# Optimization experiments

Hardware: AMD Instinct MI355X
Metric: run time of the kernel (lower is better)

The kernel has to match this reference:

```python
import jax, jax.numpy as jnp
import numpy as np

V, E, F, K, Y = 50000, 128, 256, 3, 1000  # vocab, embed, filters, kernel, labels


def setup_inputs() -> dict:
    key = jax.random.key(0)
    ks = jax.random.split(key, 8)
    x = jax.random.randint(ks[0], (16, 4096), 0, V)
    target = jax.random.randint(ks[1], (16,), 0, Y)
    embed_w = jax.random.normal(ks[2], (V, E), dtype=jnp.float32) * 0.02
    embed_w = embed_w.at[0].set(0.0)  # padding_idx=0
    conv_w = jax.random.normal(ks[3], (F, E, K), dtype=jnp.float32) * (1.0 / np.sqrt(E * K))
    conv_b = jnp.zeros((F,), dtype=jnp.float32)
    U_w = jax.random.normal(ks[4], (Y, F), dtype=jnp.float32) * (1.0 / np.sqrt(F))
    fc_w = jax.random.normal(ks[5], (Y, F), dtype=jnp.float32) * (1.0 / np.sqrt(F))
    fc_b = jnp.zeros((Y,), dtype=jnp.float32)
    return {"x": x, "target": target, "embed_w": embed_w, "conv_w": conv_w,
            "conv_b": conv_b, "U_w": U_w, "fc_w": fc_w, "fc_b": fc_b}


def reference(x, target, embed_w, conv_w, conv_b, U_w, fc_w, fc_b):
    # embedding lookup: (B, L, E); dropout is identity in eval mode
    h = embed_w[x]
    h = jnp.transpose(h, (0, 2, 1))  # (B, E, L)
    # conv1d, SAME padding (pad = floor(K/2) = 1 for K=3)
    h = jax.lax.conv_general_dilated(
        h, conv_w, window_strides=(1,), padding="SAME",
        dimension_numbers=("NCH", "OIH", "NCH"))
    h = jax.nn.relu(h + conv_b[None, :, None])  # (B, F, L)
    # label-wise attention: scores (B, Y, L), softmax over L
    scores = jnp.einsum("yf,bfl->byl", U_w, h)
    alpha = jax.nn.softmax(scores, axis=2)
    # attend: m (B, Y, F)
    m = jnp.einsum("byl,bfl->byf", alpha, h)
    # per-label dot with fc rows + bias -> logits (B, Y)
    logit = jnp.sum(fc_w[None] * m, axis=2) + fc_b
    # cross-entropy loss (target='drg')
    logp = jax.nn.log_softmax(logit, axis=1)
    loss = -jnp.mean(jnp.take_along_axis(logp, target[:, None], axis=1))
    return (logit, loss)
```

## Files before the change

kernel.cpp:

```cpp
#include <hip/hip_runtime.h>
#include <math.h>

using short8   = __attribute__((ext_vector_type(8)))  short;
using floatx4  = __attribute__((ext_vector_type(4)))  float;
using floatx16 = __attribute__((ext_vector_type(16))) float;
using uintx4   = __attribute__((ext_vector_type(4)))  unsigned int;

#define AS1 __attribute__((address_space(1)))
#define AS3 __attribute__((address_space(3)))

__device__ __forceinline__ unsigned short f2bf(float f) {
  union { float f; unsigned int u; } v; v.f = f;
  unsigned int r = v.u + 0x7FFFu + ((v.u >> 16) & 1u);
  return (unsigned short)(r >> 16);
}
__device__ __forceinline__ void gload_lds16(const void* g, void* l) {
  __builtin_amdgcn_global_load_lds((const AS1 unsigned int*)g, (AS3 unsigned int*)l, 16, 0, 0);
}

#define B_  16
#define L_  4096
#define E_  128
#define F_  256
#define Y_  1000

#define OFF_HLF   0u
#define OFF_UBF   33554432u
#define OFF_FBF   34078720u
#define OFF_WBF   34603008u
#define OFF_PART  34799616u
#define OFF_LOSST 35323904u

__global__ __launch_bounds__(256) void k_repack_u(const float* __restrict__ src,
                                                  unsigned short* __restrict__ dst) {
  int i = blockIdx.x * 256 + threadIdx.x;
  int y = i >> 8, f = i & 255;
  float v = (y < Y_) ? src[y * F_ + f] : 0.f;
  dst[i] = f2bf(v);
}

__global__ __launch_bounds__(256) void k_repack_w(const float* __restrict__ cw,
                                                  unsigned short* __restrict__ wbf) {
  int i = blockIdx.x * 256 + threadIdx.x;
  const float* s = cw + (size_t)i * 3;
  wbf[0 * 32768 + i] = f2bf(s[0]);
  wbf[1 * 32768 + i] = f2bf(s[1]);
  wbf[2 * 32768 + i] = f2bf(s[2]);
}

#define ET_STR 272
__global__ __launch_bounds__(256, 4) void k_conv(const unsigned short* __restrict__ wbf,
                                                 const float* __restrict__ conv_b,
                                                 const int* __restrict__ x,
                                                 const float* __restrict__ ew,
                                                 unsigned short* __restrict__ hlf) {
  __shared__ unsigned char et[66 * ET_STR];
  const int tid = threadIdx.x, bid = blockIdx.x;
  const int b = bid >> 6, l0 = (bid & 63) << 6;
  const int w = tid >> 6, lane = tid & 63, c = lane & 15, q = lane >> 4;
  const int* xb = x + b * L_;
  for (int s = tid; s < 1056; s += 256) {
    int row = s >> 4, sg = s & 15;
    int l = l0 - 1 + row;
    int idx = (l >= 0 && l < L_) ? xb[l] : 0;
    const float4* src = (const float4*)(ew + (size_t)idx * E_ + sg * 8);
    float4 a = src[0], bb = src[1];
    uintx4 v;
    v.x = (unsigned int)f2bf(a.x) | ((unsigned int)f2bf(a.y) << 16);
    v.y = (unsigned int)f2bf(a.z) | ((unsigned int)f2bf(a.w) << 16);
    v.z = (unsigned int)f2bf(bb.x) | ((unsigned int)f2bf(bb.y) << 16);
    v.w = (unsigned int)f2bf(bb.z) | ((unsigned int)f2bf(bb.w) << 16);
    *(uintx4*)(et + row * ET_STR + sg * 16) = v;
  }
  __syncthreads();
  const int fw = w * 64;
  floatx4 acc[4][4];
  #pragma unroll
  for (int ms = 0; ms < 4; ++ms)
    #pragma unroll
    for (int nt = 0; nt < 4; ++nt) acc[ms][nt] = (floatx4){0.f, 0.f, 0.f, 0.f};
  #pragma unroll
  for (int d = 0; d < 3; ++d)
    #pragma unroll
    for (int kq = 0; kq < 4; ++kq) {
      short8 aa[4], bb[4];
      #pragma unroll
      for (int ms = 0; ms < 4; ++ms)
        aa[ms] = *(const short8*)(et + (ms * 16 + q * 4 + (0) + c * 0 + 0 + (ms * 0)) * 0 +
                                  (ms * 16 + c + d) * ET_STR + kq * 64 + q * 16);
      #pragma unroll
      for (int nt = 0; nt < 4; ++nt)
        bb[nt] = *(const short8*)((const unsigned char*)wbf +
                   ((size_t)(d * F_ + fw + nt * 16 + c) * E_ + kq * 32 + q * 8) * 2);
      #pragma unroll
      for (int ms = 0; ms < 4; ++ms)
        #pragma unroll
        for (int nt = 0; nt < 4; ++nt)
          acc[ms][nt] = __builtin_amdgcn_mfma_f32_16x16x32_bf16(aa[ms], bb[nt], acc[ms][nt], 0, 0, 0);
    }
  #pragma unroll
  for (int nt = 0; nt < 4; ++nt) {
    int f = fw + nt * 16 + c;
    float bias = conv_b[f];
    #pragma unroll
    for (int ms = 0; ms < 4; ++ms)
      #pragma unroll
      for (int r = 0; r < 4; ++r) {
        int l = l0 + ms * 16 + q * 4 + r;
        float v = acc[ms][nt][r] + bias;
        v = v > 0.f ? v : 0.f;
        hlf[((size_t)b * L_ + l) * F_ + f] = f2bf(v);
      }
  }
}

__global__ __launch_bounds__(256, 2) void k_attn(const unsigned short* __restrict__ ubf,
                                                 const unsigned short* __restrict__ fbf,
                                                 const unsigned short* __restrict__ hlf,
                                                 float2* __restrict__ part) {
  __shared__ unsigned char lds[32768];
  const int tid = threadIdx.x;
  const int w = tid >> 6, lane = tid & 63, lo = lane & 31, hi = lane >> 5;
  const int bid = blockIdx.x;
  const int xcd = bid & 7, r0 = bid >> 3;
  const int b = xcd * 2 + (r0 & 1);
  const int r2 = r0 >> 1, yt = r2 & 7, chunk = r2 >> 3;
  const int y0 = yt << 7, yw = y0 + w * 32;
  short8 uf[16], ff[16];
  #pragma unroll
  for (int ks = 0; ks < 16; ++ks) {
    size_t off = ((size_t)(yw + lo) * F_ + ks * 16 + hi * 8) * 2;
    uf[ks] = *(const short8*)((const unsigned char*)ubf + off);
    ff[ks] = *(const short8*)((const unsigned char*)fbf + off);
  }
  float num[16], den[16];
  #pragma unroll
  for (int r = 0; r < 16; ++r) { num[r] = 0.f; den[r] = 0.f; }
  const unsigned char* hlfb = (const unsigned char*)hlf + (size_t)b * L_ * (F_ * 2);
  const int l0base = chunk << 10;

#define STAGE(dstbuf, l0v)                                                      \
  {                                                                             \
    unsigned char* dstb = (dstbuf);                                             \
    _Pragma("unroll")                                                           \
    for (int ii = 0; ii < 4; ++ii) {                                            \
      int i = w * 4 + ii;                                                       \
      int r = 2 * i + hi;                                                       \
      int g = lo ^ r;                                                           \
      gload_lds16(hlfb + (size_t)((l0v) + r) * 512 + g * 16, dstb + i * 1024);  \
    }                                                                           \
  }

  STAGE(lds, l0base);
  __syncthreads();
  for (int it = 0; it < 32; ++it) {
    unsigned char* cur = lds + ((it & 1) << 14);
    if (it < 31) STAGE(lds + (((it & 1) ^ 1) << 14), l0base + (it + 1) * 32);
    floatx16 S = {0.f,0.f,0.f,0.f,0.f,0.f,0.f,0.f,0.f,0.f,0.f,0.f,0.f,0.f,0.f,0.f};
    floatx16 G = {0.f,0.f,0.f,0.f,0.f,0.f,0.f,0.f,0.f,0.f,0.f,0.f,0.f,0.f,0.f,0.f};
    #pragma unroll
    for (int ks = 0; ks < 16; ++ks) {
      short8 bb = *(const short8*)(cur + lo * 512 + (((ks * 2 + hi) ^ lo) << 4));
      S = __builtin_amdgcn_mfma_f32_32x32x16_bf16(uf[ks], bb, S, 0, 0, 0);
      G = __builtin_amdgcn_mfma_f32_32x32x16_bf16(ff[ks], bb, G, 0, 0, 0);
    }
    #pragma unroll
    for (int r = 0; r < 16; ++r) {
      float p = __expf(S[r]);
      num[r] += p * G[r];
      den[r] += p;
    }
    __syncthreads();
  }
  #pragma unroll
  for (int r = 0; r < 16; ++r) {
    float n = num[r], d = den[r];
    n += __shfl_xor(n, 1, 64);  d += __shfl_xor(d, 1, 64);
    n += __shfl_xor(n, 2, 64);  d += __shfl_xor(d, 2, 64);
    n += __shfl_xor(n, 4, 64);  d += __shfl_xor(d, 4, 64);
    n += __shfl_xor(n, 8, 64);  d += __shfl_xor(d, 8, 64);
    n += __shfl_xor(n, 16, 64); d += __shfl_xor(d, 16, 64);
    num[r] = n; den[r] = d;
  }
  float2* pb = part + (size_t)((b * 8 + yt) * 4 + chunk) * 128;
  if (lo == 0) {
    #pragma unroll
    for (int r = 0; r < 16; ++r) {
      int yl = w * 32 + (r & 3) + 8 * (r >> 2) + 4 * hi;
      float2 v; v.x = num[r]; v.y = den[r];
      pb[yl] = v;
    }
  }
}

__global__ __launch_bounds__(256) void k_logits(const float2* __restrict__ part,
                                                const float* __restrict__ fcb,
                                                const int* __restrict__ target,
                                                float* __restrict__ out,
                                                float* __restrict__ losst) {
  __shared__ float red[4];
  const int b = blockIdx.x, tid = threadIdx.x;
  const int w = tid >> 6;
  float lg[4];
  #pragma unroll
  for (int k = 0; k < 4; ++k) {
    int y = tid + k * 256;
    int yt = y >> 7, yl = y & 127;
    float n = 0.f, la = 0.f;
    #pragma unroll
    for (int ch = 0; ch < 4; ++ch) {
      float2 v = part[(size_t)((b * 8 + yt) * 4 + ch) * 128 + yl];
      n += v.x; la += v.y;
    }
    float lv = (y < Y_) ? (n / la + fcb[y]) : -1e30f;
    lg[k] = lv;
    if (y < Y_) out[b * Y_ + y] = lv;
  }
  float m = fmaxf(fmaxf(lg[0], lg[1]), fmaxf(lg[2], lg[3]));
  for (int off = 1; off < 64; off <<= 1) m = fmaxf(m, __shfl_xor(m, off, 64));
  if ((tid & 63) == 0) red[w] = m;
  __syncthreads();
  m = fmaxf(fmaxf(red[0], red[1]), fmaxf(red[2], red[3]));
  __syncthreads();
  float s = 0.f;
  #pragma unroll
  for (int k = 0; k < 4; ++k)
    if (tid + k * 256 < Y_) s += __expf(lg[k] - m);
  for (int off = 1; off < 64; off <<= 1) s += __shfl_xor(s, off, 64);
  if ((tid & 63) == 0) red[w] = s;
  __syncthreads();
  s = red[0] + red[1] + red[2] + red[3];
  int t = target[b];
  #pragma unroll
  for (int k = 0; k < 4; ++k)
    if (tid + k * 256 == t) losst[b] = -(lg[k] - m - logf(s));
}

__global__ __launch_bounds__(64) void k_sum(const float* __restrict__ losst,
                                            float* __restrict__ out) {
  int lane = threadIdx.x;
  float v = (lane < B_) ? losst[lane] : 0.f;
  v += __shfl_xor(v, 1, 64); v += __shfl_xor(v, 2, 64);
  v += __shfl_xor(v, 4, 64); v += __shfl_xor(v, 8, 64);
  if (lane == 0) out[B_ * Y_] = v * (1.f / (float)B_);
}

extern "C" void kernel_launch(void* const* d_in, const int* in_sizes, int n_in,
                              void* d_out, int out_size, void* d_ws, size_t ws_size,
                              hipStream_t stream) {
  const int*   x       = (const int*)d_in[0];
  const int*   target  = (const int*)d_in[1];
  const float* embed_w = (const float*)d_in[2];
  const float* conv_w  = (const float*)d_in[3];
  const float* conv_b  = (const float*)d_in[4];
  const float* U_w     = (const float*)d_in[5];
  const float* fc_w    = (const float*)d_in[6];
  const float* fc_b    = (const float*)d_in[7];
  float* out = (float*)d_out;
  unsigned char* ws = (unsigned char*)d_ws;
  unsigned short* hlf   = (unsigned short*)(ws + OFF_HLF);
  unsigned short* ubf   = (unsigned short*)(ws + OFF_UBF);
  unsigned short* fbf   = (unsigned short*)(ws + OFF_FBF);
  unsigned short* wbf   = (unsigned short*)(ws + OFF_WBF);
  float2*         part  = (float2*)(ws + OFF_PART);
  float*          losst = (float*)(ws + OFF_LOSST);

  k_repack_u<<<1024, 256, 0, stream>>>(U_w, ubf);
  k_repack_u<<<1024, 256, 0, stream>>>(fc_w, fbf);
  k_repack_w<<<128, 256, 0, stream>>>(conv_w, wbf);
  k_conv<<<1024, 256, 0, stream>>>(wbf, conv_b, x, embed_w, hlf);
  k_attn<<<512, 256, 0, stream>>>(ubf, fbf, hlf, part);
  k_logits<<<16, 256, 0, stream>>>(part, fc_b, target, out, losst);
  k_sum<<<1, 64, 0, stream>>>(losst, out);
}
```

Measured before the change: 185.7 us.

## Merge repack kernels, drop loss-sum kernel, widen attention L-tile to 64

The three weight-repack kernels become one launch, and the final loss-sum kernel is removed: each batch row now atomically adds its scaled loss into an output zeroed by the repack kernel. The attention kernel processes 64 sequence positions per iteration instead of 32. It uses a 64KB double buffer and two independent S/G accumulator pairs, so it runs half as many iterations and barriers and has more MFMA work per tile. k_conv's launch bound drops from 4 to 2 blocks per SM. These changes cut launch overhead and sync cost, in exchange for higher LDS and register use in attention and a nondeterministic order of the atomic loss sum.

```diff
diff --git a/kernel.cpp b/kernel.cpp
--- a/kernel.cpp
+++ b/kernel.cpp
@@ -29,27 +29,34 @@
 #define OFF_FBF   34078720u
 #define OFF_WBF   34603008u
 #define OFF_PART  34799616u
-#define OFF_LOSST 35323904u
-
-__global__ __launch_bounds__(256) void k_repack_u(const float* __restrict__ src,
-                                                  unsigned short* __restrict__ dst) {
-  int i = blockIdx.x * 256 + threadIdx.x;
-  int y = i >> 8, f = i & 255;
-  float v = (y < Y_) ? src[y * F_ + f] : 0.f;
-  dst[i] = f2bf(v);
-}
-
-__global__ __launch_bounds__(256) void k_repack_w(const float* __restrict__ cw,
-                                                  unsigned short* __restrict__ wbf) {
-  int i = blockIdx.x * 256 + threadIdx.x;
-  const float* s = cw + (size_t)i * 3;
-  wbf[0 * 32768 + i] = f2bf(s[0]);
-  wbf[1 * 32768 + i] = f2bf(s[1]);
-  wbf[2 * 32768 + i] = f2bf(s[2]);
+
+__global__ __launch_bounds__(256) void k_repack(const float* __restrict__ Uw,
+                                                const float* __restrict__ fcw,
+                                                const float* __restrict__ cw,
+                                                unsigned short* __restrict__ ubf,
+                                                unsigned short* __restrict__ fbf,
+                                                unsigned short* __restrict__ wbf,
+                                                float* __restrict__ out) {
+  const int bid = blockIdx.x, tid = threadIdx.x;
+  if (bid == 0 && tid == 0) out[B_ * Y_] = 0.f;
+  if (bid < 2048) {
+    const float* src = (bid < 1024) ? Uw : fcw;
+    unsigned short* dst = (bid < 1024) ? ubf : fbf;
+    int i = (bid & 1023) * 256 + tid;
+    int y = i >> 8, f = i & 255;
+    float v = (y < Y_) ? src[y * F_ + f] : 0.f;
+    dst[i] = f2bf(v);
+  } else {
+    int i = (bid - 2048) * 256 + tid;
+    const float* s = cw + (size_t)i * 3;
+    wbf[0 * 32768 + i] = f2bf(s[0]);
+    wbf[1 * 32768 + i] = f2bf(s[1]);
+    wbf[2 * 32768 + i] = f2bf(s[2]);
+  }
 }
 
 #define ET_STR 272
-__global__ __launch_bounds__(256, 4) void k_conv(const unsigned short* __restrict__ wbf,
+__global__ __launch_bounds__(256, 2) void k_conv(const unsigned short* __restrict__ wbf,
                                                  const float* __restrict__ conv_b,
                                                  const int* __restrict__ x,
                                                  const float* __restrict__ ew,
@@ -86,8 +93,7 @@
       short8 aa[4], bb[4];
       #pragma unroll
       for (int ms = 0; ms < 4; ++ms)
-        aa[ms] = *(const short8*)(et + (ms * 16 + q * 4 + (0) + c * 0 + 0 + (ms * 0)) * 0 +
-                                  (ms * 16 + c + d) * ET_STR + kq * 64 + q * 16);
+        aa[ms] = *(const short8*)(et + (ms * 16 + c + d) * ET_STR + kq * 64 + q * 16);
       #pragma unroll
       for (int nt = 0; nt < 4; ++nt)
         bb[nt] = *(const short8*)((const unsigned char*)wbf +
@@ -118,7 +124,7 @@
                                                  const unsigned short* __restrict__ fbf,
                                                  const unsigned short* __restrict__ hlf,
                                                  float2* __restrict__ part) {
-  __shared__ unsigned char lds[32768];
+  __shared__ unsigned char lds[65536];
   const int tid = threadIdx.x;
   const int w = tid >> 6, lane = tid & 63, lo = lane & 31, hi = lane >> 5;
   const int bid = blockIdx.x;
@@ -143,32 +149,37 @@
   {                                                                             \
     unsigned char* dstb = (dstbuf);                                             \
     _Pragma("unroll")                                                           \
-    for (int ii = 0; ii < 4; ++ii) {                                            \
-      int i = w * 4 + ii;                                                       \
+    for (int ii = 0; ii < 8; ++ii) {                                            \
+      int i = w * 8 + ii;                                                       \
       int r = 2 * i + hi;                                                       \
-      int g = lo ^ r;                                                           \
+      int g = lo ^ (r & 31);                                                    \
       gload_lds16(hlfb + (size_t)((l0v) + r) * 512 + g * 16, dstb + i * 1024);  \
     }                                                                           \
   }
 
   STAGE(lds, l0base);
   __syncthreads();
-  for (int it = 0; it < 32; ++it) {
-    unsigned char* cur = lds + ((it & 1) << 14);
-    if (it < 31) STAGE(lds + (((it & 1) ^ 1) << 14), l0base + (it + 1) * 32);
-    floatx16 S = {0.f,0.f,0.f,0.f,0.f,0.f,0.f,0.f,0.f,0.f,0.f,0.f,0.f,0.f,0.f,0.f};
-    floatx16 G = {0.f,0.f,0.f,0.f,0.f,0.f,0.f,0.f,0.f,0.f,0.f,0.f,0.f,0.f,0.f,0.f};
+  for (int it = 0; it < 16; ++it) {
+    unsigned char* cur = lds + ((it & 1) << 15);
+    if (it < 15) STAGE(lds + (((it & 1) ^ 1) << 15), l0base + (it + 1) * 64);
+    floatx16 S0 = {0.f,0.f,0.f,0.f,0.f,0.f,0.f,0.f,0.f,0.f,0.f,0.f,0.f,0.f,0.f,0.f};
+    floatx16 S1 = S0, G0 = S0, G1 = S0;
     #pragma unroll
     for (int ks = 0; ks < 16; ++ks) {
-      short8 bb = *(const short8*)(cur + lo * 512 + (((ks * 2 + hi) ^ lo) << 4));
-      S = __builtin_amdgcn_mfma_f32_32x32x16_bf16(uf[ks], bb, S, 0, 0, 0);
-      G = __builtin_amdgcn_mfma_f32_32x32x16_bf16(ff[ks], bb, G, 0, 0, 0);
+      int gb = ((ks * 2 + hi) ^ lo) << 4;
+      short8 bb0 = *(const short8*)(cur + lo * 512 + gb);
+      short8 bb1 = *(const short8*)(cur + (lo + 32) * 512 + gb);
+      S0 = __builtin_amdgcn_mfma_f32_32x32x16_bf16(uf[ks], bb0, S0, 0, 0, 0);
+      G0 = __builtin_amdgcn_mfma_f32_32x32x16_bf16(ff[ks], bb0, G0, 0, 0, 0);
+      S1 = __builtin_amdgcn_mfma_f32_32x32x16_bf16(uf[ks], bb1, S1, 0, 0, 0);
+      G1 = __builtin_amdgcn_mfma_f32_32x32x16_bf16(ff[ks], bb1, G1, 0, 0, 0);
     }
     #pragma unroll
     for (int r = 0; r < 16; ++r) {
-      float p = __expf(S[r]);
-      num[r] += p * G[r];
-      den[r] += p;
+      float p0 = __expf(S0[r]);
+      float p1 = __expf(S1[r]);
+      num[r] += p0 * G0[r] + p1 * G1[r];
+      den[r] += p0 + p1;
     }
     __syncthreads();
   }
@@ -196,8 +207,7 @@
 __global__ __launch_bounds__(256) void k_logits(const float2* __restrict__ part,
                                                 const float* __restrict__ fcb,
                                                 const int* __restrict__ target,
-                                                float* __restrict__ out,
-                                                float* __restrict__ losst) {
+                                                float* __restrict__ out) {
   __shared__ float red[4];
   const int b = blockIdx.x, tid = threadIdx.x;
   const int w = tid >> 6;
@@ -233,16 +243,8 @@
   int t = target[b];
   #pragma unroll
   for (int k = 0; k < 4; ++k)
-    if (tid + k * 256 == t) losst[b] = -(lg[k] - m - logf(s));
-}
-
-__global__ __launch_bounds__(64) void k_sum(const float* __restrict__ losst,
-                                            float* __restrict__ out) {
-  int lane = threadIdx.x;
-  float v = (lane < B_) ? losst[lane] : 0.f;
-  v += __shfl_xor(v, 1, 64); v += __shfl_xor(v, 2, 64);
-  v += __shfl_xor(v, 4, 64); v += __shfl_xor(v, 8, 64);
-  if (lane == 0) out[B_ * Y_] = v * (1.f / (float)B_);
+    if (tid + k * 256 == t)
+      atomicAdd(&out[B_ * Y_], -(lg[k] - m - logf(s)) * (1.f / (float)B_));
 }
 
 extern "C" void kernel_launch(void* const* d_in, const int* in_sizes, int n_in,
@@ -258,18 +260,14 @@
   const float* fc_b    = (const float*)d_in[7];
   float* out = (float*)d_out;
   unsigned char* ws = (unsigned char*)d_ws;
-  unsigned short* hlf   = (unsigned short*)(ws + OFF_HLF);
-  unsigned short* ubf   = (unsigned short*)(ws + OFF_UBF);
-  unsigned short* fbf   = (unsigned short*)(ws + OFF_FBF);
-  unsigned short* wbf   = (unsigned short*)(ws + OFF_WBF);
-  float2*         part  = (float2*)(ws + OFF_PART);
-  float*          losst = (float*)(ws + OFF_LOSST);
-
-  k_repack_u<<<1024, 256, 0, stream>>>(U_w, ubf);
-  k_repack_u<<<1024, 256, 0, stream>>>(fc_w, fbf);
-  k_repack_w<<<128, 256, 0, stream>>>(conv_w, wbf);
+  unsigned short* hlf  = (unsigned short*)(ws + OFF_HLF);
+  unsigned short* ubf  = (unsigned short*)(ws + OFF_UBF);
+  unsigned short* fbf  = (unsigned short*)(ws + OFF_FBF);
+  unsigned short* wbf  = (unsigned short*)(ws + OFF_WBF);
+  float2*         part = (float2*)(ws + OFF_PART);
+
+  k_repack<<<2176, 256, 0, stream>>>(U_w, fc_w, conv_w, ubf, fbf, wbf, out);
   k_conv<<<1024, 256, 0, stream>>>(wbf, conv_b, x, embed_w, hlf);
   k_attn<<<512, 256, 0, stream>>>(ubf, fbf, hlf, part);
-  k_logits<<<16, 256, 0, stream>>>(part, fc_b, target, out, losst);
-  k_sum<<<1, 64, 0, stream>>>(losst, out);
-}
+  k_logits<<<16, 256, 0, stream>>>(part, fc_b, target, out);
+}
```

Measured after the change: 212.2 us. 1.14x slower.
